# Performance work log

Measured on AMD Instinct MI355X. Metric: run time of the kernel, lower is better.

## Reference

```python
import jax, jax.numpy as jnp
import numpy as np

D_MODEL = 4096
N_Q_HEAD = 32
N_KV_HEAD = 8
HEAD_DIM = D_MODEL // N_Q_HEAD  # 128
N_REP = N_Q_HEAD // N_KV_HEAD   # 4
B, T = 2, 2048


def _rope_tables(seq_len, head_dim, dtype=jnp.float32):
    # theta_i = 10000^(-2*(i-1)/d) for i=1..d/2  (matches torch.pow(10000, -2*(arange(1,d/2+1)-1)/d))
    i = jnp.arange(head_dim // 2, dtype=dtype)
    theta = jnp.power(10000.0, -2.0 * i / head_dim)
    angles = jnp.outer(jnp.arange(seq_len, dtype=dtype), theta)  # [T, d/2]
    return jnp.cos(angles), jnp.sin(angles)


def _apply_rope(x, cos, sin):
    # x: [B, T, h, HD]; pairs are consecutive elements (view_as_complex semantics)
    B_, T_, h, hd = x.shape
    xp = x.reshape(B_, T_, h, hd // 2, 2)
    xr, xi = xp[..., 0], xp[..., 1]
    c = cos[None, :T_, None, :]
    s = sin[None, :T_, None, :]
    out_r = xr * c - xi * s
    out_i = xr * s + xi * c
    return jnp.stack([out_r, out_i], axis=-1).reshape(B_, T_, h, hd)


def setup_inputs() -> dict:
    key = jax.random.key(0)
    ks = jax.random.split(key, 5)
    scale = 0.02
    x = jax.random.normal(ks[0], (B, T, D_MODEL), dtype=jnp.float32)
    wq = jax.random.normal(ks[1], (D_MODEL, N_Q_HEAD * HEAD_DIM), dtype=jnp.float32) * scale
    wk = jax.random.normal(ks[2], (D_MODEL, N_KV_HEAD * HEAD_DIM), dtype=jnp.float32) * scale
    wv = jax.random.normal(ks[3], (D_MODEL, N_KV_HEAD * HEAD_DIM), dtype=jnp.float32) * scale
    wo = jax.random.normal(ks[4], (N_Q_HEAD * HEAD_DIM, D_MODEL), dtype=jnp.float32) * scale
    # causal mask: 1 where masked (strict upper triangle), per masked_fill(mask==1, -inf)
    attention_mask = jnp.triu(jnp.ones((T, T), dtype=jnp.int32), k=1)
    return {"x": x, "wq": wq, "wk": wk, "wv": wv, "wo": wo, "attention_mask": attention_mask}


def reference(x, wq, wk, wv, wo, attention_mask):
    B_, T_, _ = x.shape
    xq = (x @ wq).reshape(B_, T_, N_Q_HEAD, HEAD_DIM)
    xk = (x @ wk).reshape(B_, T_, N_KV_HEAD, HEAD_DIM)
    xv = (x @ wv).reshape(B_, T_, N_KV_HEAD, HEAD_DIM)

    cos, sin = _rope_tables(T_, HEAD_DIM, x.dtype)
    xq = _apply_rope(xq, cos, sin)
    xk = _apply_rope(xk, cos, sin)

    # GQA: repeat kv heads (training path: no cache)
    xk = jnp.repeat(xk, N_REP, axis=2)  # [B, T, HQ, HD]
    xv = jnp.repeat(xv, N_REP, axis=2)

    q = xq.transpose(0, 2, 1, 3)  # [B, H, T, HD]
    k = xk.transpose(0, 2, 1, 3)
    v = xv.transpose(0, 2, 1, 3)

    scores = jnp.einsum('bhqd,bhkd->bhqk', q, k) / jnp.sqrt(jnp.asarray(HEAD_DIM, x.dtype))
    scores = jnp.where(attention_mask[None, None, :, :] == 1, -jnp.inf, scores)
    probs = jax.nn.softmax(scores, axis=-1)
    out = jnp.einsum('bhqk,bhkd->bhqd', probs, v)
    out = out.transpose(0, 2, 1, 3).reshape(B_, T_, N_Q_HEAD * HEAD_DIM)
    return out @ wo
```

## Files before the change

kernel.cpp:

```cpp
#include <hip/hip_runtime.h>
#include <hip/hip_bf16.h>
#include <math.h>

typedef __hip_bfloat16 bf16;
typedef short bf16x8 __attribute__((ext_vector_type(8)));
typedef float f32x4 __attribute__((ext_vector_type(4)));
typedef float f32x16 __attribute__((ext_vector_type(16)));
typedef unsigned int u32;
typedef unsigned short u16;

#define GLD16(g, l)                                                            \
  __builtin_amdgcn_global_load_lds(                                            \
      (const __attribute__((address_space(1))) void*)(g),                      \
      (__attribute__((address_space(3))) void*)(l), 16, 0, 0)

#define SBAR() __builtin_amdgcn_s_barrier()
#define VMCNT(n) asm volatile("s_waitcnt vmcnt(" #n ")")
#define LGKM0() asm volatile("s_waitcnt lgkmcnt(0)")

__global__ void convert_f32_bf16(const float* __restrict__ in,
                                 bf16* __restrict__ out) {
  size_t i = ((size_t)blockIdx.x * 256 + threadIdx.x) * 4;
  float4 v = *(const float4*)(in + i);
  out[i + 0] = __float2bfloat16(v.x);
  out[i + 1] = __float2bfloat16(v.y);
  out[i + 2] = __float2bfloat16(v.z);
  out[i + 3] = __float2bfloat16(v.w);
}

__global__ void transpose_f32_bf16(const float* __restrict__ in,
                                   bf16* __restrict__ out, int R, int C) {
  __shared__ bf16 tile[32][33];
  int tx = threadIdx.x & 31, ty = threadIdx.x >> 5;
  int c0 = blockIdx.x * 32, r0 = blockIdx.y * 32;
#pragma unroll
  for (int i = 0; i < 32; i += 8)
    tile[ty + i][tx] = __float2bfloat16(in[(size_t)(r0 + ty + i) * C + c0 + tx]);
  __syncthreads();
#pragma unroll
  for (int i = 0; i < 32; i += 8)
    out[(size_t)(c0 + ty + i) * R + r0 + tx] = tile[tx][ty + i];
}

__global__ void transpose_v(const bf16* __restrict__ V, bf16* __restrict__ VT) {
  __shared__ bf16 tile[32][33];
  int s = blockIdx.z, b = s >> 3, kvh = s & 7;
  int t0 = blockIdx.x * 32, d0 = blockIdx.y * 32;
  int tx = threadIdx.x & 31, ty = threadIdx.x >> 5;
#pragma unroll
  for (int i = 0; i < 32; i += 8)
    tile[ty + i][tx] =
        V[(size_t)(b * 2048 + t0 + ty + i) * 6144 + kvh * 128 + d0 + tx];
  __syncthreads();
#pragma unroll
  for (int i = 0; i < 32; i += 8)
    VT[((size_t)s * 128 + d0 + ty + i) * 2048 + t0 + tx] = tile[tx][ty + i];
}

__global__ void rope_table_k(float* __restrict__ tab) {
  int idx = blockIdx.x * 256 + threadIdx.x;
  int t = idx >> 6, i = idx & 63;
  float theta = powf(10000.0f, -2.0f * (float)i / 128.0f);
  float ang = (float)t * theta;
  tab[idx * 2 + 0] = cosf(ang);
  tab[idx * 2 + 1] = sinf(ang);
}

__global__ void rope_apply(bf16* __restrict__ X, const float* __restrict__ tab,
                           int nheads, int rowstride, float omul) {
  size_t idx = (size_t)blockIdx.x * 256 + threadIdx.x;
  int i = (int)(idx & 63);
  size_t rest = idx >> 6;
  int h = (int)(rest % nheads);
  size_t r = rest / nheads;
  int t = (int)(r & 2047);
  float c = tab[(t * 64 + i) * 2 + 0];
  float s = tab[(t * 64 + i) * 2 + 1];
  bf16* p = X + r * (size_t)rowstride + h * 128 + 2 * i;
  float xr = __bfloat162float(p[0]), xi = __bfloat162float(p[1]);
  p[0] = __float2bfloat16((xr * c - xi * s) * omul);
  p[1] = __float2bfloat16((xr * s + xi * c) * omul);
}

template <typename OutT>
__global__ __launch_bounds__(512, 2) void gemm_bt8(const bf16* __restrict__ A,
                                                   const bf16* __restrict__ BT,
                                                   OutT* __restrict__ C, int M,
                                                   int N, int K) {
  __shared__ bf16 AS[2][2][128 * 64];
  __shared__ bf16 BS[2][2][128 * 64];

  const int tid = threadIdx.x;
  const int lane = tid & 63;
  const int w = tid >> 6, wm = w >> 2, wn = w & 3;
  const int lr = lane & 15, hi = lane >> 4;

  int gx = gridDim.x;
  int nwg = gx * gridDim.y;
  int bid = blockIdx.y * gx + blockIdx.x;
  int swz = (bid & 7) * (nwg >> 3) + (bid >> 3);
  const int m0 = (swz / gx) * 256, n0 = (swz % gx) * 256;

  const int NKT = K >> 6;
  const int NI = K >> 7;
  const int srow = tid >> 3;
  const int scol = ((tid & 7) ^ (srow & 7)) << 3;

  f32x4 acc[8][4];
#pragma unroll
  for (int m = 0; m < 8; ++m)
#pragma unroll
    for (int n = 0; n < 4; ++n)
#pragma unroll
      for (int j = 0; j < 4; ++j) acc[m][n][j] = 0.f;

  auto STAGE_A = [&](int buf, int kt) {
    int kk0 = (kt < NKT) ? kt * 64 : 0;
#pragma unroll
    for (int hs = 0; hs < 4; ++hs) {
      int ha = hs >> 1, sa = hs & 1;
      const bf16* g = A + (size_t)(m0 + ha * 128 + sa * 64 + srow) * K + kk0 + scol;
      GLD16(g, &AS[buf][ha][(sa * 64 + srow) * 64 + (tid & 7) * 8]);
    }
  };
  auto STAGE_B = [&](int buf, int kt, int half) {
    int kk0 = (kt < NKT) ? kt * 64 : 0;
#pragma unroll
    for (int sa = 0; sa < 2; ++sa) {
      const bf16* g =
          BT + (size_t)(n0 + half * 128 + sa * 64 + srow) * K + kk0 + scol;
      GLD16(g, &BS[buf][half][(sa * 64 + srow) * 64 + (tid & 7) * 8]);
    }
  };

  bf16x8 bfr[4][2], af[2][2];
  auto READ_B = [&](int buf) {
#pragma unroll
    for (int n = 0; n < 4; ++n) {
      int row = (wn & 1) * 64 + n * 16 + lr;
#pragma unroll
      for (int kk = 0; kk < 2; ++kk)
        bfr[n][kk] = *(const bf16x8*)(&BS[buf][wn >> 1]
                                         [row * 64 + (((kk * 4 + hi) ^ (row & 7)) << 3)]);
    }
  };
  auto READ_A = [&](int buf, int q) {
#pragma unroll
    for (int mm = 0; mm < 2; ++mm) {
      int row = (q * 2 + mm) * 16 + lr;
#pragma unroll
      for (int kk = 0; kk < 2; ++kk)
        af[mm][kk] = *(const bf16x8*)(&AS[buf][wm]
                                         [row * 64 + (((kk * 4 + hi) ^ (row & 7)) << 3)]);
    }
  };

#define MFMA16(q)                                                              \
  do {                                                                         \
    LGKM0();                                                                   \
    __builtin_amdgcn_s_setprio(1);                                             \
    _Pragma("unroll") for (int mm = 0; mm < 2; ++mm)                           \
        _Pragma("unroll") for (int n = 0; n < 4; ++n)                          \
        _Pragma("unroll") for (int kk = 0; kk < 2; ++kk)                       \
            acc[(q) * 2 + mm][n] = __builtin_amdgcn_mfma_f32_16x16x32_bf16(    \
                af[mm][kk], bfr[n][kk], acc[(q) * 2 + mm][n], 0, 0, 0);        \
    __builtin_amdgcn_s_setprio(0);                                             \
  } while (0)

  STAGE_A(0, 0);
  STAGE_B(0, 0, 0);
  STAGE_B(0, 0, 1);
  STAGE_B(1, 1, 0);
  STAGE_B(1, 1, 1);
  VMCNT(4);
  SBAR();

  for (int i = 0; i < NI; ++i) {
    int t = 2 * i;
    READ_B(0); READ_A(0, 0); STAGE_A(1, t + 1);
    SBAR(); MFMA16(0); SBAR();
    READ_A(0, 1); STAGE_B(0, t + 2, 0);
    SBAR(); MFMA16(1); SBAR();
    READ_A(0, 2); STAGE_B(0, t + 2, 1);
    SBAR(); MFMA16(2); SBAR();
    READ_A(0, 3);
    SBAR(); MFMA16(3); VMCNT(4); SBAR();
    READ_B(1); READ_A(1, 0); STAGE_A(0, t + 2);
    SBAR(); MFMA16(0); SBAR();
    READ_A(1, 1); STAGE_B(1, t + 3, 0);
    SBAR(); MFMA16(1); SBAR();
    READ_A(1, 2); STAGE_B(1, t + 3, 1);
    SBAR(); MFMA16(2); SBAR();
    READ_A(1, 3);
    SBAR(); MFMA16(3); VMCNT(4); SBAR();
  }

  VMCNT(0);
  SBAR();

#pragma unroll
  for (int m = 0; m < 8; ++m) {
    int row_base = m0 + wm * 128 + m * 16 + hi * 4;
#pragma unroll
    for (int n = 0; n < 4; ++n) {
      int col = n0 + wn * 64 + n * 16 + lr;
#pragma unroll
      for (int j = 0; j < 4; ++j) {
        float v = acc[m][n][j];
        if constexpr (sizeof(OutT) == 2)
          C[(size_t)(row_base + j) * N + col] = (OutT)__float2bfloat16(v);
        else
          C[(size_t)(row_base + j) * N + col] = (OutT)v;
      }
    }
  }
#undef MFMA16
}

static __device__ inline u32 cvtpk_bf16(float a, float b) {
  u32 r;
  asm("v_cvt_pk_bf16_f32 %0, %1, %2" : "=v"(r) : "v"(a), "v"(b));
  return r;
}

__global__ __launch_bounds__(512) void flash_attn3(const bf16* __restrict__ Q,
                                                   const bf16* __restrict__ K,
                                                   const bf16* __restrict__ VT,
                                                   bf16* __restrict__ AO) {
  __shared__ bf16 Kbuf[2][64 * 128];
  __shared__ bf16 Vbuf[2][128 * 64];

  int bid = blockIdx.x;
  int b = bid >> 8;
  int i = (bid >> 3) & 31;
  int kvh = bid & 7;
  int hq = i >> 3;
  int qt = 7 - (i & 7);
  int h = kvh * 4 + hq;

  const int tid = threadIdx.x;
  const int lane = tid & 63, w = tid >> 6;
  const int ql = lane & 31, hi = lane >> 5;
  const int qrow0 = qt * 256 + w * 32;
  const int nt = 4 * qt + 4;

  const bf16* Kg0 = K + (size_t)b * 2048 * 6144 + kvh * 128;
  const bf16* Vg0 = VT + (size_t)(b * 8 + kvh) * 128 * 2048;

  bf16x8 qf[8];
  {
    const bf16* qb =
        Q + (size_t)(b * 2048 + qrow0 + ql) * 6144 + h * 128 + hi * 8;
#pragma unroll
    for (int dc = 0; dc < 8; ++dc) qf[dc] = *(const bf16x8*)(qb + dc * 16);
  }

  f32x16 O[4];
#pragma unroll
  for (int d4 = 0; d4 < 4; ++d4)
#pragma unroll
    for (int e = 0; e < 16; ++e) O[d4][e] = 0.f;
  float m_ = -1e30f, l_ = 0.f;

  auto STAGE = [&](int buf, int kv0) {
    bf16* Ks = &Kbuf[buf][0];
    bf16* Vs = &Vbuf[buf][0];
    const bf16* Kg = Kg0 + (size_t)kv0 * 6144;
    const bf16* Vg = Vg0 + kv0;
#pragma unroll
    for (int it = 0; it < 2; ++it) {
      int s = it * 512 + tid;
      int row = s >> 4, c = s & 15;
      GLD16(Kg + (size_t)row * 6144 + ((c ^ (row & 7)) << 3), Ks + s * 8);
    }
#pragma unroll
    for (int it = 0; it < 2; ++it) {
      int s = it * 512 + tid;
      int row = s >> 3, c = s & 7;
      GLD16(Vg + (size_t)row * 2048 + ((c ^ (row & 7)) << 3), Vs + s * 8);
    }
  };

  STAGE(0, 0);
  __syncthreads();

  for (int t = 0; t < nt; ++t) {
    int kv0 = t * 64;
    if (t + 1 < nt) STAGE((t + 1) & 1, kv0 + 64);

    if (kv0 <= qrow0 + 31) {
      const bf16* Ks = &Kbuf[t & 1][0];
      const bf16* Vs = &Vbuf[t & 1][0];

      f32x16 Sx[2];
#pragma unroll
      for (int cb = 0; cb < 2; ++cb)
#pragma unroll
        for (int e = 0; e < 16; ++e) Sx[cb][e] = 0.f;

      __builtin_amdgcn_s_setprio(1);
#pragma unroll
      for (int cb = 0; cb < 2; ++cb) {
        int krow = cb * 32 + ql;
#pragma unroll
        for (int dc = 0; dc < 8; ++dc) {
          bf16x8 kf = *(const bf16x8*)(Ks + krow * 128 +
                                       (((dc * 2 + hi) ^ (ql & 7)) << 3));
          Sx[cb] = __builtin_amdgcn_mfma_f32_32x32x16_bf16(kf, qf[dc], Sx[cb],
                                                           0, 0, 0);
        }
      }
      __builtin_amdgcn_s_setprio(0);

      int q = qrow0 + ql;
      bool domask = (kv0 + 63 > qrow0);
      if (domask) {
#pragma unroll
        for (int cb = 0; cb < 2; ++cb)
#pragma unroll
          for (int r = 0; r < 16; ++r) {
            int kv = kv0 + cb * 32 + (r & 3) + 8 * (r >> 2) + 4 * hi;
            if (kv > q) Sx[cb][r] = -1e30f;
          }
      }
      float pm = -1e30f;
#pragma unroll
      for (int cb = 0; cb < 2; ++cb)
#pragma unroll
        for (int r = 0; r < 16; ++r) pm = fmaxf(pm, Sx[cb][r]);
      pm = fmaxf(pm, __shfl_xor(pm, 32));

      if (!__all(pm - m_ <= 11.5416f)) {
        float nm = fmaxf(m_, pm);
        float rs = exp2f(m_ - nm);
        m_ = nm;
        l_ *= rs;
#pragma unroll
        for (int d4 = 0; d4 < 4; ++d4)
#pragma unroll
          for (int e = 0; e < 16; ++e) O[d4][e] *= rs;
      }
      float ps = 0.f;
#pragma unroll
      for (int cb = 0; cb < 2; ++cb)
#pragma unroll
        for (int r = 0; r < 16; ++r) {
          float p = exp2f(Sx[cb][r] - m_);
          Sx[cb][r] = p;
          ps += p;
        }
      ps += __shfl_xor(ps, 32);
      l_ += ps;

      bf16x8 pb[4];
#pragma unroll
      for (int kb = 0; kb < 4; ++kb) {
        int cb = kb >> 1, r0 = 8 * (kb & 1);
        u32 Av = cvtpk_bf16(Sx[cb][r0 + 0], Sx[cb][r0 + 1]);
        u32 Bv = cvtpk_bf16(Sx[cb][r0 + 2], Sx[cb][r0 + 3]);
        u32 Cv = cvtpk_bf16(Sx[cb][r0 + 4], Sx[cb][r0 + 5]);
        u32 Dv = cvtpk_bf16(Sx[cb][r0 + 6], Sx[cb][r0 + 7]);
        u32 sA = (u32)__shfl_xor((int)Av, 32);
        u32 sB = (u32)__shfl_xor((int)Bv, 32);
        u32 sC = (u32)__shfl_xor((int)Cv, 32);
        u32 sD = (u32)__shfl_xor((int)Dv, 32);
        union { u32 u[4]; bf16x8 v; } pk;
        pk.u[0] = hi ? sC : Av;
        pk.u[1] = hi ? sD : Bv;
        pk.u[2] = hi ? Cv : sA;
        pk.u[3] = hi ? Dv : sB;
        pb[kb] = pk.v;
      }

      __builtin_amdgcn_s_setprio(1);
#pragma unroll
      for (int d4 = 0; d4 < 4; ++d4) {
        int vrow = d4 * 32 + ql;
#pragma unroll
        for (int kb = 0; kb < 4; ++kb) {
          bf16x8 vf = *(const bf16x8*)(Vs + vrow * 64 +
                                       (((kb * 2 + hi) ^ (ql & 7)) << 3));
          O[d4] = __builtin_amdgcn_mfma_f32_32x32x16_bf16(vf, pb[kb], O[d4], 0,
                                                          0, 0);
        }
      }
      __builtin_amdgcn_s_setprio(0);
    }
    __syncthreads();
  }

  float inv = 1.0f / l_;
  bf16* outp = AO + (size_t)(b * 2048 + qrow0 + ql) * 4096 + h * 128;
#pragma unroll
  for (int d4 = 0; d4 < 4; ++d4)
#pragma unroll
    for (int rg = 0; rg < 4; ++rg) {
      union { u16 s[4]; unsigned long long v; } pk;
#pragma unroll
      for (int j = 0; j < 4; ++j)
        pk.s[j] = __bfloat16_as_ushort(__float2bfloat16(O[d4][rg * 4 + j] * inv));
      *(unsigned long long*)(outp + d4 * 32 + rg * 8 + hi * 4) = pk.v;
    }
}

extern "C" void kernel_launch(void* const* d_in, const int* in_sizes, int n_in,
                              void* d_out, int out_size, void* d_ws,
                              size_t ws_size, hipStream_t stream) {
  const float* x = (const float*)d_in[0];
  const float* wq = (const float*)d_in[1];
  const float* wk = (const float*)d_in[2];
  const float* wv = (const float*)d_in[3];
  const float* wo = (const float*)d_in[4];

  char* ws = (char*)d_ws;
  bf16* xb    = (bf16*)(ws + 0);
  bf16* WqkvT = (bf16*)(ws + 33554432);
  bf16* WoT   = (bf16*)(ws + 83886080);
  bf16* QKV   = (bf16*)(ws + 117440512);
  bf16* VTb   = (bf16*)(ws + 167772160);
  float* tab  = (float*)(ws + 176160768);
  bf16* AOb   = xb;

  const float LOG2E = 1.4426950408889634f;
  const float ISQ = 0.08838834764831845f;

  convert_f32_bf16<<<16384, 256, 0, stream>>>(x, xb);
  transpose_f32_bf16<<<dim3(128, 128), 256, 0, stream>>>(wq, WqkvT, 4096, 4096);
  transpose_f32_bf16<<<dim3(32, 128), 256, 0, stream>>>(
      wk, WqkvT + (size_t)4096 * 4096, 4096, 1024);
  transpose_f32_bf16<<<dim3(32, 128), 256, 0, stream>>>(
      wv, WqkvT + (size_t)5120 * 4096, 4096, 1024);
  transpose_f32_bf16<<<dim3(128, 128), 256, 0, stream>>>(wo, WoT, 4096, 4096);
  rope_table_k<<<512, 256, 0, stream>>>(tab);

  gemm_bt8<bf16><<<dim3(24, 16), 512, 0, stream>>>(xb, WqkvT, QKV, 4096, 6144,
                                                   4096);

  rope_apply<<<32768, 256, 0, stream>>>(QKV, tab, 32, 6144, LOG2E * ISQ);
  rope_apply<<<8192, 256, 0, stream>>>(QKV + 4096, tab, 8, 6144, 1.0f);

  transpose_v<<<dim3(64, 4, 16), 256, 0, stream>>>(QKV + 5120, VTb);

  flash_attn3<<<512, 512, 0, stream>>>(QKV, QKV + 4096, VTb, AOb);

  gemm_bt8<float><<<dim3(16, 16), 512, 0, stream>>>(AOb, WoT, (float*)d_out,
                                                    4096, 4096, 4096);
}
```

Measured before the change: 619.5 us.

## Fuse Q RoPE into attention load and double-buffer A fragments in GEMM

Removes the separate rope_apply pass over Q. The attention kernel now reads the cos/sin table and applies the rotation plus the softmax scale while loading its Q fragments, which saves a full read-modify-write of Q in global memory. Separately, the GEMM main loop now reads two A fragment groups at a time into separate registers. This halves the number of barrier and lgkmcnt wait pairs per k-step, at the cost of more registers. The Q rounding path changes slightly: Q is rounded to bf16, rotated in fp32, then rounded again, as the old rope_apply presumably did too.

```diff
diff --git a/kernel.cpp b/kernel.cpp
--- a/kernel.cpp
+++ b/kernel.cpp
@@ -133,7 +133,7 @@
     }
   };
 
-  bf16x8 bfr[4][2], af[2][2];
+  bf16x8 bfr[4][2], afA[2][2], afB[2][2];
   auto READ_B = [&](int buf) {
 #pragma unroll
     for (int n = 0; n < 4; ++n) {
@@ -144,55 +144,60 @@
                                          [row * 64 + (((kk * 4 + hi) ^ (row & 7)) << 3)]);
     }
   };
-  auto READ_A = [&](int buf, int q) {
+  auto READ_A_TO = [&](bf16x8(&dst)[2][2], int buf, int q) {
 #pragma unroll
     for (int mm = 0; mm < 2; ++mm) {
       int row = (q * 2 + mm) * 16 + lr;
 #pragma unroll
       for (int kk = 0; kk < 2; ++kk)
-        af[mm][kk] = *(const bf16x8*)(&AS[buf][wm]
-                                         [row * 64 + (((kk * 4 + hi) ^ (row & 7)) << 3)]);
+        dst[mm][kk] = *(const bf16x8*)(&AS[buf][wm]
+                                          [row * 64 + (((kk * 4 + hi) ^ (row & 7)) << 3)]);
     }
   };
 
-#define MFMA16(q)                                                              \
+#define MFMA16(q, AF)                                                          \
   do {                                                                         \
-    LGKM0();                                                                   \
-    __builtin_amdgcn_s_setprio(1);                                             \
     _Pragma("unroll") for (int mm = 0; mm < 2; ++mm)                           \
         _Pragma("unroll") for (int n = 0; n < 4; ++n)                          \
         _Pragma("unroll") for (int kk = 0; kk < 2; ++kk)                       \
             acc[(q) * 2 + mm][n] = __builtin_amdgcn_mfma_f32_16x16x32_bf16(    \
-                af[mm][kk], bfr[n][kk], acc[(q) * 2 + mm][n], 0, 0, 0);        \
-    __builtin_amdgcn_s_setprio(0);                                             \
+                AF[mm][kk], bfr[n][kk], acc[(q) * 2 + mm][n], 0, 0, 0);        \
   } while (0)
 
   STAGE_A(0, 0);
-  STAGE_B(0, 0, 0);
-  STAGE_B(0, 0, 1);
-  STAGE_B(1, 1, 0);
-  STAGE_B(1, 1, 1);
+  STAGE_B(0, 0, 0); STAGE_B(0, 0, 1);
+  STAGE_B(1, 1, 0); STAGE_B(1, 1, 1);
   VMCNT(4);
   SBAR();
 
   for (int i = 0; i < NI; ++i) {
     int t = 2 * i;
-    READ_B(0); READ_A(0, 0); STAGE_A(1, t + 1);
-    SBAR(); MFMA16(0); SBAR();
-    READ_A(0, 1); STAGE_B(0, t + 2, 0);
-    SBAR(); MFMA16(1); SBAR();
-    READ_A(0, 2); STAGE_B(0, t + 2, 1);
-    SBAR(); MFMA16(2); SBAR();
-    READ_A(0, 3);
-    SBAR(); MFMA16(3); VMCNT(4); SBAR();
-    READ_B(1); READ_A(1, 0); STAGE_A(0, t + 2);
-    SBAR(); MFMA16(0); SBAR();
-    READ_A(1, 1); STAGE_B(1, t + 3, 0);
-    SBAR(); MFMA16(1); SBAR();
-    READ_A(1, 2); STAGE_B(1, t + 3, 1);
-    SBAR(); MFMA16(2); SBAR();
-    READ_A(1, 3);
-    SBAR(); MFMA16(3); VMCNT(4); SBAR();
+    READ_B(0); READ_A_TO(afA, 0, 0); READ_A_TO(afB, 0, 1);
+    STAGE_A(1, t + 1);
+    SBAR(); LGKM0();
+    __builtin_amdgcn_s_setprio(1); MFMA16(0, afA); MFMA16(1, afB);
+    __builtin_amdgcn_s_setprio(0);
+    SBAR();
+    READ_A_TO(afA, 0, 2); READ_A_TO(afB, 0, 3);
+    STAGE_B(0, t + 2, 0); STAGE_B(0, t + 2, 1);
+    SBAR(); LGKM0();
+    __builtin_amdgcn_s_setprio(1); MFMA16(2, afA); MFMA16(3, afB);
+    __builtin_amdgcn_s_setprio(0);
+    VMCNT(4);
+    SBAR();
+    READ_B(1); READ_A_TO(afA, 1, 0); READ_A_TO(afB, 1, 1);
+    STAGE_A(0, t + 2);
+    SBAR(); LGKM0();
+    __builtin_amdgcn_s_setprio(1); MFMA16(0, afA); MFMA16(1, afB);
+    __builtin_amdgcn_s_setprio(0);
+    SBAR();
+    READ_A_TO(afA, 1, 2); READ_A_TO(afB, 1, 3);
+    STAGE_B(1, t + 3, 0); STAGE_B(1, t + 3, 1);
+    SBAR(); LGKM0();
+    __builtin_amdgcn_s_setprio(1); MFMA16(2, afA); MFMA16(3, afB);
+    __builtin_amdgcn_s_setprio(0);
+    VMCNT(4);
+    SBAR();
   }
 
   VMCNT(0);
@@ -226,6 +231,7 @@
 __global__ __launch_bounds__(512) void flash_attn3(const bf16* __restrict__ Q,
                                                    const bf16* __restrict__ K,
                                                    const bf16* __restrict__ VT,
+                                                   const float* __restrict__ tab,
                                                    bf16* __restrict__ AO) {
   __shared__ bf16 Kbuf[2][64 * 128];
   __shared__ bf16 Vbuf[2][128 * 64];
@@ -249,10 +255,26 @@
 
   bf16x8 qf[8];
   {
-    const bf16* qb =
-        Q + (size_t)(b * 2048 + qrow0 + ql) * 6144 + h * 128 + hi * 8;
-#pragma unroll
-    for (int dc = 0; dc < 8; ++dc) qf[dc] = *(const bf16x8*)(qb + dc * 16);
+    int tpos = qrow0 + ql;
+    const bf16* qb = Q + (size_t)(b * 2048 + tpos) * 6144 + h * 128 + hi * 8;
+    const float* tb = tab + (size_t)tpos * 128;
+    const float QS = 1.4426950408889634f * 0.08838834764831845f;
+#pragma unroll
+    for (int dc = 0; dc < 8; ++dc) {
+      union { bf16x8 v; u16 s[8]; } in;
+      in.v = *(const bf16x8*)(qb + dc * 16);
+      union { u32 u[4]; bf16x8 v; } o;
+#pragma unroll
+      for (int p = 0; p < 4; ++p) {
+        int ii = dc * 8 + hi * 4 + p;
+        float2 cs = *(const float2*)(tb + 2 * ii);
+        float xr = __uint_as_float((u32)in.s[2 * p] << 16);
+        float xi = __uint_as_float((u32)in.s[2 * p + 1] << 16);
+        o.u[p] = cvtpk_bf16((xr * cs.x - xi * cs.y) * QS,
+                            (xr * cs.y + xi * cs.x) * QS);
+      }
+      qf[dc] = o.v;
+    }
   }
 
   f32x16 O[4];
@@ -421,9 +443,6 @@
   float* tab  = (float*)(ws + 176160768);
   bf16* AOb   = xb;
 
-  const float LOG2E = 1.4426950408889634f;
-  const float ISQ = 0.08838834764831845f;
-
   convert_f32_bf16<<<16384, 256, 0, stream>>>(x, xb);
   transpose_f32_bf16<<<dim3(128, 128), 256, 0, stream>>>(wq, WqkvT, 4096, 4096);
   transpose_f32_bf16<<<dim3(32, 128), 256, 0, stream>>>(
@@ -436,12 +455,11 @@
   gemm_bt8<bf16><<<dim3(24, 16), 512, 0, stream>>>(xb, WqkvT, QKV, 4096, 6144,
                                                    4096);
 
-  rope_apply<<<32768, 256, 0, stream>>>(QKV, tab, 32, 6144, LOG2E * ISQ);
   rope_apply<<<8192, 256, 0, stream>>>(QKV + 4096, tab, 8, 6144, 1.0f);
 
   transpose_v<<<dim3(64, 4, 16), 256, 0, stream>>>(QKV + 5120, VTb);
 
-  flash_attn3<<<512, 512, 0, stream>>>(QKV, QKV + 4096, VTb, AOb);
+  flash_attn3<<<512, 512, 0, stream>>>(QKV, QKV + 4096, VTb, tab, AOb);
 
   gemm_bt8<float><<<dim3(16, 16), 512, 0, stream>>>(AOb, WoT, (float*)d_out,
                                                     4096, 4096, 4096);
```

Measured after the change: 608.0 us. About the same (-1.9%).
